# Kernel tuning notes

Hardware: AMD Instinct MI355X
Metric: run time of the kernel (lower is better)

Reference implementation:

```python
import jax, jax.numpy as jnp
import numpy as np

N_HEADS = 32
N_KV_HEADS = 8
HEAD_DIM = 64
DIM = 2048
MAX_CTX = 2048
N_REP = N_HEADS // N_KV_HEADS


def setup_inputs() -> dict:
    key = jax.random.key(0)
    ks = jax.random.split(key, 8)
    B, S = 1, 2048
    x = jax.random.normal(ks[0], (B, S, DIM), dtype=jnp.float32)
    # RoPE frequencies (real cos/sin, [S, head_dim//2])
    inv_freq = 1.0 / (10000.0 ** (np.arange(0, HEAD_DIM, 2, dtype=np.float32) / HEAD_DIM))
    t = np.arange(S, dtype=np.float32)
    freqs = np.outer(t, inv_freq)  # [S, HEAD_DIM//2]
    freqs_cos = jnp.asarray(np.cos(freqs), dtype=jnp.float32)
    freqs_sin = jnp.asarray(np.sin(freqs), dtype=jnp.float32)
    input_pos = jnp.arange(S, dtype=jnp.int32)
    scale = 0.02
    wq = jax.random.normal(ks[1], (N_HEADS * HEAD_DIM, DIM), dtype=jnp.float32) * scale
    wk = jax.random.normal(ks[2], (N_KV_HEADS * HEAD_DIM, DIM), dtype=jnp.float32) * scale
    wv = jax.random.normal(ks[3], (N_KV_HEADS * HEAD_DIM, DIM), dtype=jnp.float32) * scale
    wo = jax.random.normal(ks[4], (DIM, N_HEADS * HEAD_DIM), dtype=jnp.float32) * scale
    k_cache = jnp.zeros((B, N_KV_HEADS, MAX_CTX, HEAD_DIM), dtype=jnp.float32)
    v_cache = jnp.zeros((B, N_KV_HEADS, MAX_CTX, HEAD_DIM), dtype=jnp.float32)
    return {"x": x, "freqs_cos": freqs_cos, "freqs_sin": freqs_sin,
            "input_pos": input_pos, "wq": wq, "wk": wk, "wv": wv, "wo": wo,
            "k_cache": k_cache, "v_cache": v_cache}


def _apply_rope(x, cos, sin):
    # x: [B, S, H, HEAD_DIM]; cos/sin: [S, HEAD_DIM//2]
    xr = x[..., 0::2]
    xi = x[..., 1::2]
    c = cos[None, :, None, :]
    s = sin[None, :, None, :]
    out_r = xr * c - xi * s
    out_i = xr * s + xi * c
    # interleave back: stack on new trailing axis then flatten pairs
    out = jnp.stack([out_r, out_i], axis=-1)
    return out.reshape(x.shape)


def reference(x, freqs_cos, freqs_sin, input_pos, wq, wk, wv, wo, k_cache, v_cache):
    B, S, _ = x.shape
    q = (x @ wq.T).reshape(B, S, N_HEADS, HEAD_DIM)
    k = (x @ wk.T).reshape(B, S, N_KV_HEADS, HEAD_DIM)
    v = (x @ wv.T).reshape(B, S, N_KV_HEADS, HEAD_DIM)
    q = _apply_rope(q, freqs_cos, freqs_sin)
    k = _apply_rope(k, freqs_cos, freqs_sin)
    q = q.transpose(0, 2, 1, 3)   # [B, H, S, D]
    k = k.transpose(0, 2, 1, 3)   # [B, KV, S, D]
    v = v.transpose(0, 2, 1, 3)
    # KV-cache scatter update at input_pos
    k_full = k_cache.at[:, :, input_pos].set(k)   # [B, KV, MAX_CTX, D]
    v_full = v_cache.at[:, :, input_pos].set(v)
    # causal mask rows gathered at input_pos: [S, MAX_CTX]
    causal = jnp.tril(jnp.ones((MAX_CTX, MAX_CTX), dtype=bool))
    attn_mask = causal[input_pos]
    # GQA repeat_interleave along head dim
    k_rep = jnp.repeat(k_full, N_REP, axis=1)    # [B, H, MAX_CTX, D]
    v_rep = jnp.repeat(v_full, N_REP, axis=1)
    scale = 1.0 / jnp.sqrt(jnp.asarray(HEAD_DIM, dtype=x.dtype))
    scores = jnp.einsum('bhsd,bhtd->bhst', q, k_rep) * scale  # [B, H, S, MAX_CTX]
    neg = jnp.asarray(jnp.finfo(scores.dtype).min, dtype=scores.dtype)
    scores = jnp.where(attn_mask[None, None, :, :], scores, neg)
    attn = jax.nn.softmax(scores, axis=-1)
    y = jnp.einsum('bhst,bhtd->bhsd', attn, v_rep)  # [B, H, S, D]
    y = y.transpose(0, 2, 1, 3).reshape(B, S, N_HEADS * HEAD_DIM)
    return y @ wo.T
```

## Files before the change

kernel.cpp:

```cpp
#include <hip/hip_runtime.h>


typedef __attribute__((ext_vector_type(8))) __bf16 bf16x8;
typedef __attribute__((ext_vector_type(4))) float f32x4;

#define S_LEN 2048
#define DIMN  2048
#define NH    32
#define NKV   8
#define HD    64
#define QKVF  3072

struct DoPair { static constexpr bool value = true; };
struct OnlyB  { static constexpr bool value = false; };

__device__ __forceinline__ ushort f2bf(float f) {
  union { float f; unsigned u; } v; v.f = f;
  unsigned r = v.u + 0x7fffu + ((v.u >> 16) & 1u);
  return (ushort)(r >> 16);
}
__device__ __forceinline__ unsigned pack_bf2_rz(float a, float b) {
  union { float f; unsigned u; } va, vb; va.f = a; vb.f = b;
  return (va.u >> 16) | (vb.u & 0xffff0000u);
}
__device__ __forceinline__ float bf2f(ushort u) {
  union { unsigned u; float f; } v; v.u = ((unsigned)u) << 16;
  return v.f;
}
__device__ __forceinline__ void gld_lds16(const void* g, void* l) {
  __builtin_amdgcn_global_load_lds(
      (const __attribute__((address_space(1))) unsigned int*)g,
      (__attribute__((address_space(3))) unsigned int*)l, 16, 0, 0);
}

__global__ __launch_bounds__(256) void convert_all(
    const float* __restrict__ x, const float* __restrict__ wq,
    const float* __restrict__ wk, const float* __restrict__ wv,
    const float* __restrict__ wo, ushort* __restrict__ xb,
    ushort* __restrict__ wqkvb, ushort* __restrict__ wob) {
  const size_t NX = 4u * 1024 * 1024;
  const size_t NK = 1024 * 1024;
  size_t idx = ((size_t)blockIdx.x * 256 + threadIdx.x) * 4;
  const float* src; ushort* dst;
  if (idx < NX)                { src = x  + idx;                  dst = xb + idx; }
  else if (idx < 2 * NX)       { src = wq + (idx - NX);           dst = wqkvb + (idx - NX); }
  else if (idx < 2 * NX + NK)  { src = wk + (idx - 2 * NX);       dst = wqkvb + NX + (idx - 2 * NX); }
  else if (idx < 2 * NX + 2*NK){ src = wv + (idx - 2 * NX - NK);  dst = wqkvb + NX + NK + (idx - 2 * NX - NK); }
  else                         { src = wo + (idx - 2 * NX - 2*NK);dst = wob + (idx - 2 * NX - 2 * NK); }
  float4 v = *(const float4*)src;
  ushort4 o; o.x = f2bf(v.x); o.y = f2bf(v.y); o.z = f2bf(v.z); o.w = f2bf(v.w);
  *(ushort4*)dst = o;
}

template <int OUT_BF16, int BM, int BN>
__global__ __launch_bounds__(256) void gemm_bt(
    const ushort* __restrict__ A, const ushort* __restrict__ B,
    void* __restrict__ Cv, int M, int N, int K) {
  constexpr int IB = BM / 32;
  constexpr int JB = BN / 32;
  constexpr int NGA = BM / 8;
  constexpr int GPW = (BM + BN) / 32;
  __shared__ __align__(16) ushort As[2][BM * 64];
  __shared__ __align__(16) ushort Bs[2][BN * 64];
  const int n0 = blockIdx.x * BN, m0 = blockIdx.y * BM;
  const int t = threadIdx.x;
  const int lane = t & 63, wave = t >> 6;
  const int wm = (wave >> 1) * (BM / 2), wn = (wave & 1) * (BN / 2);
  const int col = lane & 15, quad = lane >> 4;
  const int sw = col & 7;
  const int lrow = lane >> 3;
  const int scol = ((lane & 7) ^ lrow) * 8;
  f32x4 acc[IB][JB] = {};

  auto stage = [&](int b, int kk) {
#pragma unroll
    for (int c = 0; c < GPW; ++c) {
      int g = wave * GPW + c;
      if (g < NGA)
        gld_lds16(&A[(size_t)(m0 + g * 8 + lrow) * K + kk + scol], &As[b][g * 8 * 64]);
      else
        gld_lds16(&B[(size_t)(n0 + (g - NGA) * 8 + lrow) * K + kk + scol],
                  &Bs[b][(g - NGA) * 8 * 64]);
    }
  };

  stage(0, 0);
  __syncthreads();
  for (int kk = 0; kk < K; kk += 64) {
    const int b = (kk >> 6) & 1;
    if (kk + 64 < K) stage(b ^ 1, kk + 64);
#pragma unroll
    for (int c = 0; c < 2; ++c) {
      const int chs = ((c * 4 + quad) ^ sw) * 8;
      bf16x8 af[IB], bfr[JB];
#pragma unroll
      for (int i = 0; i < IB; ++i)
        af[i] = *(const bf16x8*)&As[b][(wm + i * 16 + col) * 64 + chs];
#pragma unroll
      for (int j = 0; j < JB; ++j)
        bfr[j] = *(const bf16x8*)&Bs[b][(wn + j * 16 + col) * 64 + chs];
#pragma unroll
      for (int i = 0; i < IB; ++i)
#pragma unroll
        for (int j = 0; j < JB; ++j)
          acc[i][j] = __builtin_amdgcn_mfma_f32_16x16x32_bf16(af[i], bfr[j], acc[i][j], 0, 0, 0);
    }
    __syncthreads();
  }
#pragma unroll
  for (int i = 0; i < IB; ++i)
#pragma unroll
    for (int r = 0; r < 4; ++r) {
      int m = m0 + wm + i * 16 + quad * 4 + r;
      if (OUT_BF16) {
        ushort* C = (ushort*)Cv;
#pragma unroll
        for (int j = 0; j < JB; ++j)
          C[(size_t)m * N + n0 + wn + j * 16 + col] = f2bf(acc[i][j][r]);
      } else {
        float* C = (float*)Cv;
#pragma unroll
        for (int j = 0; j < JB; ++j)
          C[(size_t)m * N + n0 + wn + j * 16 + col] = acc[i][j][r];
      }
    }
}

__global__ __launch_bounds__(256) void rope_layout(
    const ushort* __restrict__ qkv, const float* __restrict__ fc,
    const float* __restrict__ fs, ushort* __restrict__ qb,
    ushort* __restrict__ kb, ushort* __restrict__ vt) {
  __shared__ ushort T[64][72];
  const int hh = blockIdx.x;
  const int s0 = blockIdx.y * 256;
  const int t = threadIdx.x;
  if (hh < 32) {
    ushort* dst = qb + (size_t)hh * S_LEN * 64;
    const float qs = 0.18033688011112042f;
    const int sr = t >> 4, dc = (t & 15) * 4, i0 = (t & 15) * 2;
#pragma unroll 4
    for (int pass = 0; pass < 16; ++pass) {
      int s = s0 + pass * 16 + sr;
      ushort4 vv = *(const ushort4*)&qkv[(size_t)s * QKVF + hh * 64 + dc];
      float2 cc = *(const float2*)&fc[s * 32 + i0];
      float2 ss = *(const float2*)&fs[s * 32 + i0];
      float xr0 = bf2f(vv.x), xi0 = bf2f(vv.y), xr1 = bf2f(vv.z), xi1 = bf2f(vv.w);
      ushort4 ov;
      ov.x = f2bf((xr0 * cc.x - xi0 * ss.x) * qs); ov.y = f2bf((xr0 * ss.x + xi0 * cc.x) * qs);
      ov.z = f2bf((xr1 * cc.y - xi1 * ss.y) * qs); ov.w = f2bf((xr1 * ss.y + xi1 * cc.y) * qs);
      *(ushort4*)&dst[(size_t)s * 64 + dc] = ov;
    }
  } else if (hh < 40) {
    const int kh2 = hh - 32;
    const int sr8 = t >> 3;
    const int ch = t & 7;
#pragma unroll 2
    for (int pass = 0; pass < 8; ++pass) {
      int s = s0 + pass * 32 + sr8;
      ushort in[8], out[8];
      *(int4*)&in[0] = *(const int4*)&qkv[(size_t)s * QKVF + 2048 + kh2 * 64 + ch * 8];
      float4 cc = *(const float4*)&fc[s * 32 + ch * 4];
      float4 ss4 = *(const float4*)&fs[s * 32 + ch * 4];
      const float* cp = &cc.x; const float* sp = &ss4.x;
#pragma unroll
      for (int i = 0; i < 4; ++i) {
        float xr = bf2f(in[2 * i]), xi = bf2f(in[2 * i + 1]);
        out[2 * i]     = f2bf(xr * cp[i] - xi * sp[i]);
        out[2 * i + 1] = f2bf(xr * sp[i] + xi * cp[i]);
      }
      int r = s & 63, tile = s >> 6;
      size_t pos = ((size_t)(kh2 * 32 + tile)) * 4096 +
                   ((size_t)(((ch >> 2) * 4 + (r >> 4)) * 64 + (ch & 3) * 16 + (r & 15))) * 8;
      *(int4*)&kb[pos] = *(const int4*)&out[0];
    }
  } else {
    const int vh = hh - 40;
    for (int sub = 0; sub < 4; ++sub) {
      int sb = s0 + sub * 64;
      int sr = t >> 2, dc = (t & 3) * 16;
      ushort tmp[16];
      *(int4*)&tmp[0] = *(const int4*)&qkv[(size_t)(sb + sr) * QKVF + 2560 + vh * 64 + dc];
      *(int4*)&tmp[8] = *(const int4*)&qkv[(size_t)(sb + sr) * QKVF + 2560 + vh * 64 + dc + 8];
      __syncthreads();
      const int pcol = ((sr & 15) << 2) | (sr >> 4);
#pragma unroll
      for (int k = 0; k < 16; ++k) T[dc + k][pcol] = tmp[k];
      __syncthreads();
      int d = t >> 2;
      int ch0 = (t & 3) * 2, ch1 = ch0 + 1;
      int tile = sb >> 6;
      size_t base = ((size_t)(vh * 32 + tile)) * 4096;
      size_t p0 = base + ((size_t)(((ch0 >> 2) * 4 + (d >> 4)) * 64 + (ch0 & 3) * 16 + (d & 15))) * 8;
      size_t p1 = base + ((size_t)(((ch1 >> 2) * 4 + (d >> 4)) * 64 + (ch1 & 3) * 16 + (d & 15))) * 8;
      *(int4*)&vt[p0] = *(const int4*)&T[d][ch0 * 8];
      *(int4*)&vt[p1] = *(const int4*)&T[d][ch1 * 8];
    }
  }
}

__global__ __launch_bounds__(256, 2) void attn(
    const ushort* __restrict__ qbg, const ushort* __restrict__ kbg,
    const ushort* __restrict__ vtg, ushort* __restrict__ yb) {
  __shared__ __align__(16) ushort Ps[4][2][16][64];
  const int kvh = blockIdx.x;
  const int y = blockIdx.y;
  const int sA = y, sB = 127 - y;
  const int ntA = (sA >> 2) + 1;
  const int ntB = (sB >> 2) + 1;
  const int wave = threadIdx.x >> 6;
  const int lane = threadIdx.x & 63;
  const int col = lane & 15, quad = lane >> 4;
  const int h = kvh * 4 + wave;
  const ushort* qh = qbg + (size_t)h * S_LEN * HD;
  const ushort* kbase = kbg + (size_t)kvh * 32 * 4096;
  const ushort* vbase = vtg + (size_t)kvh * 32 * 4096;

  const int q0A = sA * 16, q0B = sB * 16;
  bf16x8 qfA[2], qfB[2];
  qfA[0] = *(const bf16x8*)&qh[(size_t)(q0A + col) * HD + quad * 8];
  qfA[1] = *(const bf16x8*)&qh[(size_t)(q0A + col) * HD + 32 + quad * 8];
  qfB[0] = *(const bf16x8*)&qh[(size_t)(q0B + col) * HD + quad * 8];
  qfB[1] = *(const bf16x8*)&qh[(size_t)(q0B + col) * HD + 32 + quad * 8];
  float lA[4] = {}, lB[4] = {};
  f32x4 oA[4] = {}, oB[4] = {};

  bf16x8 k0[8], k1[8];

  auto loadK = [&](bf16x8 (&kf)[8], int t) {
    const ushort* kt = kbase + (size_t)t * 4096;
#pragma unroll
    for (int p = 0; p < 8; ++p) kf[p] = *(const bf16x8*)&kt[(p * 64 + lane) * 8];
  };

  auto body = [&](bf16x8 (&kfc)[8], bf16x8 (&kfn)[8], int t) {
    const bool doA = (t < ntA);
    const bool maskA = (t == ntA - 1);
    const bool maskB = (t == ntB - 1);
    bf16x8 vf[8];
    const ushort* vtt = vbase + (size_t)t * 4096;
#pragma unroll
    for (int p = 0; p < 8; ++p) vf[p] = *(const bf16x8*)&vtt[(p * 64 + lane) * 8];
    if (t + 1 < ntB) loadK(kfn, t + 1);
    __builtin_amdgcn_sched_barrier(0);
    f32x4 scA[4] = {}, scB[4] = {};
#pragma unroll
    for (int c = 0; c < 2; ++c)
#pragma unroll
      for (int j = 0; j < 4; ++j)
        scB[j] = __builtin_amdgcn_mfma_f32_16x16x32_bf16(qfB[c], kfc[c * 4 + j], scB[j], 0, 0, 0);
    if (doA) {
#pragma unroll
      for (int c = 0; c < 2; ++c)
#pragma unroll
        for (int j = 0; j < 4; ++j)
          scA[j] = __builtin_amdgcn_mfma_f32_16x16x32_bf16(qfA[c], kfc[c * 4 + j], scA[j], 0, 0, 0);
    }
#pragma unroll
    for (int r = 0; r < 4; ++r) {
      const int prow = quad * 4 + r;
      const int psw = (((col >> 1) ^ (prow & 7)) << 3) + ((col & 1) << 2);
      const int rowq = q0B + prow;
      float pr[4];
#pragma unroll
      for (int j = 0; j < 4; ++j) {
        float e = __builtin_amdgcn_exp2f(scB[j][r]);
        if (maskB) e = (t * 64 + j * 16 + col > rowq) ? 0.f : e;
        pr[j] = e;
      }
      lB[r] += (pr[0] + pr[1]) + (pr[2] + pr[3]);
      uint2 pk;
      pk.x = pack_bf2_rz(pr[0], pr[1]);
      pk.y = pack_bf2_rz(pr[2], pr[3]);
      *(uint2*)&Ps[wave][1][prow][psw] = pk;
    }
    if (doA) {
#pragma unroll
      for (int r = 0; r < 4; ++r) {
        const int prow = quad * 4 + r;
        const int psw = (((col >> 1) ^ (prow & 7)) << 3) + ((col & 1) << 2);
        const int rowq = q0A + prow;
        float pr[4];
#pragma unroll
        for (int j = 0; j < 4; ++j) {
          float e = __builtin_amdgcn_exp2f(scA[j][r]);
          if (maskA) e = (t * 64 + j * 16 + col > rowq) ? 0.f : e;
          pr[j] = e;
        }
        lA[r] += (pr[0] + pr[1]) + (pr[2] + pr[3]);
        uint2 pk;
        pk.x = pack_bf2_rz(pr[0], pr[1]);
        pk.y = pack_bf2_rz(pr[2], pr[3]);
        *(uint2*)&Ps[wave][0][prow][psw] = pk;
      }
    }
#pragma unroll
    for (int c = 0; c < 2; ++c) {
      const int psr = ((c * 4 + quad) ^ (col & 7)) * 8;
      bf16x8 pfB = *(const bf16x8*)&Ps[wave][1][col][psr];
#pragma unroll
      for (int db = 0; db < 4; ++db)
        oB[db] = __builtin_amdgcn_mfma_f32_16x16x32_bf16(pfB, vf[c * 4 + db], oB[db], 0, 0, 0);
    }
    if (doA) {
#pragma unroll
      for (int c = 0; c < 2; ++c) {
        const int psr = ((c * 4 + quad) ^ (col & 7)) * 8;
        bf16x8 pfA = *(const bf16x8*)&Ps[wave][0][col][psr];
#pragma unroll
        for (int db = 0; db < 4; ++db)
          oA[db] = __builtin_amdgcn_mfma_f32_16x16x32_bf16(pfA, vf[c * 4 + db], oA[db], 0, 0, 0);
      }
    }
  };

  loadK(k0, 0);
  for (int t = 0; t < ntB;) {
    body(k0, k1, t);
    ++t;
    if (t >= ntB) break;
    body(k1, k0, t);
    ++t;
  }

  auto write_out = [&](const f32x4 (&o)[4], const float (&l)[4], int q0) {
#pragma unroll
    for (int r = 0; r < 4; ++r) {
      float ls = l[r];
      ls += __shfl_xor(ls, 1);
      ls += __shfl_xor(ls, 2);
      ls += __shfl_xor(ls, 4);
      ls += __shfl_xor(ls, 8);
      float inv = 1.0f / ls;
      int rowq = q0 + quad * 4 + r;
#pragma unroll
      for (int db = 0; db < 4; ++db)
        yb[(size_t)rowq * (NH * HD) + h * HD + db * 16 + col] = f2bf(o[db][r] * inv);
    }
  };
  write_out(oA, lA, q0A);
  write_out(oB, lB, q0B);
}

extern "C" void kernel_launch(void* const* d_in, const int* in_sizes, int n_in,
                              void* d_out, int out_size, void* d_ws, size_t ws_size,
                              hipStream_t stream) {
  (void)in_sizes; (void)n_in; (void)out_size; (void)ws_size;
  const float* x  = (const float*)d_in[0];
  const float* fc = (const float*)d_in[1];
  const float* fs = (const float*)d_in[2];
  const float* wq = (const float*)d_in[4];
  const float* wk = (const float*)d_in[5];
  const float* wv = (const float*)d_in[6];
  const float* wo = (const float*)d_in[7];
  ushort* w = (ushort*)d_ws;
  const size_t M1 = 1024 * 1024;
  ushort* xb    = w;
  ushort* wqkvb = w + 4 * M1;
  ushort* wob   = w + 10 * M1;
  ushort* qkvb  = w + 14 * M1;
  ushort* qb    = w + 20 * M1;
  ushort* kb    = w + 24 * M1;
  ushort* vt    = w + 25 * M1;
  ushort* yb    = w + 26 * M1;

  convert_all<<<14336, 256, 0, stream>>>(x, wq, wk, wv, wo, xb, wqkvb, wob);
  gemm_bt<1, 128, 96><<<dim3(QKVF / 96, S_LEN / 128), 256, 0, stream>>>(xb, wqkvb, qkvb, S_LEN, QKVF, DIMN);
  rope_layout<<<dim3(48, 8), 256, 0, stream>>>(qkvb, fc, fs, qb, kb, vt);
  attn<<<dim3(NKV, 64), 256, 0, stream>>>(qb, kb, vt, yb);
  gemm_bt<0, 64, 128><<<dim3(DIMN / 128, S_LEN / 64), 256, 0, stream>>>(yb, wob, d_out, S_LEN, DIMN, NH * HD);
}
```

Before: 212.8 us.

## Software-pipeline attention so P·V of previous tile overlaps current QK

The attention loop is restructured so each iteration issues the P·V MFMAs for the previous key tile while the current tile's K and V loads are in flight, before computing the current QK scores and softmax. P tiles are double-buffered in LDS by iteration parity, and the V fragments rotate between two register sets, with a final P·V drain for the B query strip after the loop. The intent is to hide global load latency and the exp/pack work behind matrix instructions. In exchange, the cross-iteration K prefetch is dropped, so K is loaded in the same iteration that uses it, and register pressure and LDS use grow.

```diff
diff --git a/kernel.cpp b/kernel.cpp
--- a/kernel.cpp
+++ b/kernel.cpp
@@ -10,9 +10,6 @@
 #define NKV   8
 #define HD    64
 #define QKVF  3072
-
-struct DoPair { static constexpr bool value = true; };
-struct OnlyB  { static constexpr bool value = false; };
 
 __device__ __forceinline__ ushort f2bf(float f) {
   union { float f; unsigned u; } v; v.f = f;
@@ -201,7 +198,7 @@
 __global__ __launch_bounds__(256, 2) void attn(
     const ushort* __restrict__ qbg, const ushort* __restrict__ kbg,
     const ushort* __restrict__ vtg, ushort* __restrict__ yb) {
-  __shared__ __align__(16) ushort Ps[4][2][16][64];
+  __shared__ __align__(16) ushort Ps[4][2][2][16][64];
   const int kvh = blockIdx.x;
   const int y = blockIdx.y;
   const int sA = y, sB = 127 - y;
@@ -224,36 +221,48 @@
   float lA[4] = {}, lB[4] = {};
   f32x4 oA[4] = {}, oB[4] = {};
 
-  bf16x8 k0[8], k1[8];
-
-  auto loadK = [&](bf16x8 (&kf)[8], int t) {
-    const ushort* kt = kbase + (size_t)t * 4096;
-#pragma unroll
-    for (int p = 0; p < 8; ++p) kf[p] = *(const bf16x8*)&kt[(p * 64 + lane) * 8];
+  bf16x8 v0[8], v1[8];
+
+  auto pv = [&](f32x4 (&o)[4], int par, int strip, bf16x8 (&vfp)[8]) {
+#pragma unroll
+    for (int c = 0; c < 2; ++c) {
+      const int psr = ((c * 4 + quad) ^ (col & 7)) * 8;
+      bf16x8 pf = *(const bf16x8*)&Ps[wave][par][strip][col][psr];
+#pragma unroll
+      for (int db = 0; db < 4; ++db)
+        o[db] = __builtin_amdgcn_mfma_f32_16x16x32_bf16(pf, vfp[c * 4 + db], o[db], 0, 0, 0);
+    }
   };
 
-  auto body = [&](bf16x8 (&kfc)[8], bf16x8 (&kfn)[8], int t) {
+  auto body = [&](bf16x8 (&vfc)[8], bf16x8 (&vfp)[8], int t) {
     const bool doA = (t < ntA);
     const bool maskA = (t == ntA - 1);
     const bool maskB = (t == ntB - 1);
-    bf16x8 vf[8];
+    const int par = t & 1, pp = par ^ 1;
+    bf16x8 kf[8];
+    const ushort* kt = kbase + (size_t)t * 4096;
+#pragma unroll
+    for (int p = 0; p < 8; ++p) kf[p] = *(const bf16x8*)&kt[(p * 64 + lane) * 8];
     const ushort* vtt = vbase + (size_t)t * 4096;
 #pragma unroll
-    for (int p = 0; p < 8; ++p) vf[p] = *(const bf16x8*)&vtt[(p * 64 + lane) * 8];
-    if (t + 1 < ntB) loadK(kfn, t + 1);
+    for (int p = 0; p < 8; ++p) vfc[p] = *(const bf16x8*)&vtt[(p * 64 + lane) * 8];
     __builtin_amdgcn_sched_barrier(0);
+    if (t > 0) {
+      pv(oB, pp, 1, vfp);
+      if (t - 1 < ntA) pv(oA, pp, 0, vfp);
+    }
     f32x4 scA[4] = {}, scB[4] = {};
 #pragma unroll
     for (int c = 0; c < 2; ++c)
 #pragma unroll
       for (int j = 0; j < 4; ++j)
-        scB[j] = __builtin_amdgcn_mfma_f32_16x16x32_bf16(qfB[c], kfc[c * 4 + j], scB[j], 0, 0, 0);
+        scB[j] = __builtin_amdgcn_mfma_f32_16x16x32_bf16(qfB[c], kf[c * 4 + j], scB[j], 0, 0, 0);
     if (doA) {
 #pragma unroll
       for (int c = 0; c < 2; ++c)
 #pragma unroll
         for (int j = 0; j < 4; ++j)
-          scA[j] = __builtin_amdgcn_mfma_f32_16x16x32_bf16(qfA[c], kfc[c * 4 + j], scA[j], 0, 0, 0);
+          scA[j] = __builtin_amdgcn_mfma_f32_16x16x32_bf16(qfA[c], kf[c * 4 + j], scA[j], 0, 0, 0);
     }
 #pragma unroll
     for (int r = 0; r < 4; ++r) {
@@ -271,7 +280,7 @@
       uint2 pk;
       pk.x = pack_bf2_rz(pr[0], pr[1]);
       pk.y = pack_bf2_rz(pr[2], pr[3]);
-      *(uint2*)&Ps[wave][1][prow][psw] = pk;
+      *(uint2*)&Ps[wave][par][1][prow][psw] = pk;
     }
     if (doA) {
 #pragma unroll
@@ -290,36 +299,26 @@
         uint2 pk;
         pk.x = pack_bf2_rz(pr[0], pr[1]);
         pk.y = pack_bf2_rz(pr[2], pr[3]);
-        *(uint2*)&Ps[wave][0][prow][psw] = pk;
+        *(uint2*)&Ps[wave][par][0][prow][psw] = pk;
       }
     }
-#pragma unroll
-    for (int c = 0; c < 2; ++c) {
-      const int psr = ((c * 4 + quad) ^ (col & 7)) * 8;
-      bf16x8 pfB = *(const bf16x8*)&Ps[wave][1][col][psr];
-#pragma unroll
-      for (int db = 0; db < 4; ++db)
-        oB[db] = __builtin_amdgcn_mfma_f32_16x16x32_bf16(pfB, vf[c * 4 + db], oB[db], 0, 0, 0);
-    }
-    if (doA) {
-#pragma unroll
-      for (int c = 0; c < 2; ++c) {
-        const int psr = ((c * 4 + quad) ^ (col & 7)) * 8;
-        bf16x8 pfA = *(const bf16x8*)&Ps[wave][0][col][psr];
-#pragma unroll
-        for (int db = 0; db < 4; ++db)
-          oA[db] = __builtin_amdgcn_mfma_f32_16x16x32_bf16(pfA, vf[c * 4 + db], oA[db], 0, 0, 0);
-      }
-    }
   };
 
-  loadK(k0, 0);
-  for (int t = 0; t < ntB;) {
-    body(k0, k1, t);
-    ++t;
-    if (t >= ntB) break;
-    body(k1, k0, t);
-    ++t;
+  {
+    int t = 0;
+    for (;;) {
+      body(v0, v1, t);
+      ++t;
+      if (t >= ntB) break;
+      body(v1, v0, t);
+      ++t;
+      if (t >= ntB) break;
+    }
+  }
+  {
+    const int lp = (ntB - 1) & 1;
+    if (lp == 0) pv(oB, 0, 1, v0);
+    else         pv(oB, 1, 1, v1);
   }
 
   auto write_out = [&](const f32x4 (&o)[4], const float (&l)[4], int q0) {
```

Measured after the change: 228.9 us. 7.6% more time.
